# Performance work log

Hardware: AMD Instinct MI355X
Metric: run time of the kernel (lower is better)

Reference implementation:

```python
import jax, jax.numpy as jnp
import numpy as np

L = 4000      # num identities
C = 8         # num cameras; center bank is label-major: center j -> (label j//C, cam j%C)
T = 0.07      # temperature
HARD_NEG_K = 50
LAMDA = 0.5


def setup_inputs() -> dict:
    key = jax.random.key(0)
    k1, k2, k3, k4 = jax.random.split(key, 4)
    n, d = 256, 2048
    feats = jax.random.normal(k1, (n, d), dtype=jnp.float32)
    centers = jax.random.normal(k2, (L * C, d), dtype=jnp.float32)
    centers = centers / jnp.linalg.norm(centers, axis=1, keepdims=True)  # bank is kept unit-norm
    labels = jax.random.randint(k3, (n,), 0, L, dtype=jnp.int64)
    camids = jax.random.randint(k4, (n,), 0, C, dtype=jnp.int64)
    return {"feats": feats, "centers": centers, "labels": labels, "camids": camids, "epoch": 5}


def _cap_losses(feats, centers, labels, camids):
    n = feats.shape[0]
    M = centers.shape[0]
    feats = feats / jnp.linalg.norm(feats, axis=1, keepdims=True)  # F.normalize(p=2, dim=1)
    center_labels = jnp.arange(M) // C
    center_cams = jnp.arange(M) % C

    sims = jnp.einsum('nd,md->nm', feats, centers) / T  # [n, M] scaled similarities
    own_idx = labels * C + camids                        # cam_label_index[(label, cam)]
    own = sims[jnp.arange(n), own_idx]                   # numerator logits
    exp_sims = jnp.exp(sims)                             # unit vectors => sims <= 1/T ~ 14.3, safe

    # ---- intra-camera loss: denominator over centers sharing the sample's camid ----
    cam_mask = (center_cams[None, :] == camids[:, None])
    denom_intra = jnp.sum(exp_sims * cam_mask, axis=1)
    loss_i = own - jnp.log(denom_intra)                  # log(frac_up/frac_down)
    # mean per camid, then sum over camids present in the batch, negated
    ones = jnp.ones((n,), dtype=feats.dtype)
    cam_sums = jax.ops.segment_sum(loss_i, camids, num_segments=C)
    cam_cnts = jax.ops.segment_sum(ones, camids, num_segments=C)
    loss_intra = -jnp.sum(jnp.where(cam_cnts > 0, cam_sums / jnp.maximum(cam_cnts, 1.0), 0.0))

    # ---- inter loss: same-label centers + first-K hard negatives (in bank order) ----
    lbl_mask = (center_labels[None, :] == labels[:, None])
    other = ~lbl_mask
    # torch concatenates other-label centers in label order and takes the FIRST 50 (a slice,
    # not top-k); label-major bank order makes that = first 50 other-label centers by index.
    rank = jnp.cumsum(other.astype(jnp.int32), axis=1)
    hard_mask = other & (rank <= HARD_NEG_K)
    denom_inter = jnp.sum(exp_sims * lbl_mask, axis=1) + jnp.sum(exp_sims * hard_mask, axis=1)
    loss_j = own - jnp.log(denom_inter)
    lbl_sums = jax.ops.segment_sum(loss_j, labels, num_segments=L)
    lbl_cnts = jax.ops.segment_sum(ones, labels, num_segments=L)
    loss_inter = -jnp.sum(jnp.where(lbl_cnts > 0, lbl_sums / jnp.maximum(lbl_cnts, 1.0), 0.0))

    return loss_intra, loss_inter


def reference(feats, centers, labels, camids, epoch):
    loss_intra, loss_inter = _cap_losses(feats, centers, labels, camids)
    if epoch < 5:  # epoch is a static python int
        return loss_intra
    return jnp.stack([loss_intra, LAMDA * loss_inter])
```

## Files before the change

### kernel.cpp

```cpp
#include <hip/hip_runtime.h>

typedef __attribute__((ext_vector_type(8))) __bf16 bf16x8;
typedef __attribute__((ext_vector_type(4))) __bf16 bf16x4;
typedef __attribute__((ext_vector_type(4))) float f32x4;

#define N_SAMP 256
#define DIM    2048
#define NCENT  32000
#define INV_T  14.285714285714285714f
#define NWG    500

__global__ __launch_bounds__(256) void norm_kernel(const float* __restrict__ feats,
                                                   __bf16* __restrict__ fnorm,
                                                   float* __restrict__ d_acc) {
    int row = blockIdx.x;
    int tid = threadIdx.x;
    if (row < 16) d_acc[row * 256 + tid] = 0.f;
    const float* src = feats + (size_t)row * DIM;
    float4 v0 = reinterpret_cast<const float4*>(src)[2 * tid];
    float4 v1 = reinterpret_cast<const float4*>(src)[2 * tid + 1];
    float ss = v0.x * v0.x + v0.y * v0.y + v0.z * v0.z + v0.w * v0.w
             + v1.x * v1.x + v1.y * v1.y + v1.z * v1.z + v1.w * v1.w;
    #pragma unroll
    for (int off = 1; off < 64; off <<= 1) ss += __shfl_xor(ss, off, 64);
    __shared__ float wsum[4];
    if ((tid & 63) == 0) wsum[tid >> 6] = ss;
    __syncthreads();
    float inv = 1.0f / sqrtf(wsum[0] + wsum[1] + wsum[2] + wsum[3]);
    bf16x8 o;
    o[0] = (__bf16)(v0.x * inv); o[1] = (__bf16)(v0.y * inv);
    o[2] = (__bf16)(v0.z * inv); o[3] = (__bf16)(v0.w * inv);
    o[4] = (__bf16)(v1.x * inv); o[5] = (__bf16)(v1.y * inv);
    o[6] = (__bf16)(v1.z * inv); o[7] = (__bf16)(v1.w * inv);
    *reinterpret_cast<bf16x8*>(fnorm + (size_t)row * DIM + tid * 8) = o;
}

__global__ __launch_bounds__(512, 4) void sims_kernel(
    const __bf16* __restrict__ fnorm, const float* __restrict__ centers,
    const int* __restrict__ labels, const int* __restrict__ camids,
    float* __restrict__ d_acc, float* __restrict__ d_own)
{
    __shared__ __align__(16) char sA[2][8192];
    __shared__ __align__(16) char sB[2][8192];

    const int tid  = threadIdx.x;
    const int wave = tid >> 6;
    const int lane = tid & 63;
    const int l15  = lane & 15;
    const int lhi  = lane >> 4;

    const int d   = blockIdx.x;
    const int xcd = d & 7, loc = d >> 3;
    const int lid = (xcd < 4 ? xcd * 63 : 252 + (xcd - 4) * 62) + loc;
    const int nb  = lid >> 1;
    const int mb  = lid & 1;

    const int wr = (wave >> 2) * 64;
    const int wc = (wave & 3) * 32;

    f32x4 acc[4][2] = {};

    const float4* bsrc = reinterpret_cast<const float4*>(centers);
    const uint4*  asrc = reinterpret_cast<const uint4*>(fnorm);

    auto issue = [&](int step, float4& b0, float4& b1, uint4& a) {
        int r0 = tid >> 3, p0 = tid & 7;
        b0 = bsrc[(size_t)(nb * 128 + r0) * 512 + step * 8 + p0];
        int r1 = (512 + tid) >> 3, p1 = tid & 7;
        b1 = bsrc[(size_t)(nb * 128 + r1) * 512 + step * 8 + p1];
        int ra = tid >> 2, pa = tid & 3;
        a = asrc[(size_t)(mb * 128 + ra) * 256 + step * 4 + pa];
    };
    auto wrbuf = [&](int b, const float4& b0, const float4& b1, const uint4& a) {
        #pragma unroll
        for (int j = 0; j < 2; ++j) {
            const float4& v = j ? b1 : b0;
            int row = (j * 512 + tid) >> 3, pos = tid & 7;
            int adr = (row * 64 + pos * 8) ^ ((row & 7) << 4);
            bf16x4 o;
            o[0] = (__bf16)v.x; o[1] = (__bf16)v.y;
            o[2] = (__bf16)v.z; o[3] = (__bf16)v.w;
            *reinterpret_cast<uint2*>(&sB[b][adr]) = __builtin_bit_cast(uint2, o);
        }
        {
            int row = tid >> 2, pos = tid & 3;
            int adr = (row * 64 + pos * 16) ^ ((row & 7) << 4);
            *reinterpret_cast<uint4*>(&sA[b][adr]) = a;
        }
    };
    auto compute = [&](int b) {
        bf16x8 af[4], bf[2];
        #pragma unroll
        for (int mi = 0; mi < 4; ++mi) {
            int row = wr + mi * 16 + l15;
            int adr = (row * 64 + lhi * 16) ^ ((row & 7) << 4);
            af[mi] = *reinterpret_cast<const bf16x8*>(&sA[b][adr]);
        }
        #pragma unroll
        for (int ni = 0; ni < 2; ++ni) {
            int row = wc + ni * 16 + l15;
            int adr = (row * 64 + lhi * 16) ^ ((row & 7) << 4);
            bf[ni] = *reinterpret_cast<const bf16x8*>(&sB[b][adr]);
        }
        #pragma unroll
        for (int mi = 0; mi < 4; ++mi)
            #pragma unroll
            for (int ni = 0; ni < 2; ++ni)
                acc[mi][ni] = __builtin_amdgcn_mfma_f32_16x16x32_bf16(
                    af[mi], bf[ni], acc[mi][ni], 0, 0, 0);
    };
    #define BAR() do { asm volatile("s_waitcnt lgkmcnt(0)" ::: "memory"); \
                       __builtin_amdgcn_s_barrier(); } while (0)

    float4 b0A, b1A; uint4 aA;
    float4 b0B, b1B; uint4 aB;

    issue(0, b0A, b1A, aA);
    issue(1, b0B, b1B, aB);
    wrbuf(0, b0A, b1A, aA);
    BAR();
    for (int t = 0; t < 64; t += 2) {
        if (t + 2 < 64) issue(t + 2, b0A, b1A, aA);
        compute(0);
        wrbuf(1, b0B, b1B, aB);
        BAR();
        if (t + 3 < 64) issue(t + 3, b0B, b1B, aB);
        compute(1);
        if (t + 2 < 64) {
            wrbuf(0, b0A, b1A, aA);
            BAR();
        }
    }

    float* slot = d_acc + (d & 7) * 512;
    #pragma unroll
    for (int mi = 0; mi < 4; ++mi) {
        #pragma unroll
        for (int r = 0; r < 4; ++r) {
            int i   = mb * 128 + wr + mi * 16 + lhi * 4 + r;
            int lab = labels[i], cam = camids[i];
            int oidx = lab * 8 + cam;
            float pi = 0.f, pj = 0.f;
            #pragma unroll
            for (int ni = 0; ni < 2; ++ni) {
                int c = nb * 128 + wc + ni * 16 + l15;
                float s = acc[mi][ni][r] * INV_T;
                float e = __expf(s);
                if ((l15 & 7) == cam) pi += e;
                bool ol = ((c >> 3) == lab);
                bool hard = (!ol) && (c < ((c < lab * 8) ? 50 : 58));
                if (ol || hard) pj += e;
                if (c == oidx) d_own[i] = s;
            }
            #pragma unroll
            for (int off = 1; off < 16; off <<= 1) {
                pi += __shfl_xor(pi, off, 64);
                pj += __shfl_xor(pj, off, 64);
            }
            if (l15 == 0) {
                atomicAdd(&slot[i], pi);
                atomicAdd(&slot[N_SAMP + i], pj);
            }
        }
    }
}

__global__ __launch_bounds__(256) void finalize_kernel(
    const float* __restrict__ d_acc, const float* __restrict__ d_own,
    const int* __restrict__ labels, const int* __restrict__ camids,
    float* __restrict__ out, int out_size)
{
    __shared__ int s_lab[N_SAMP], s_cam[N_SAMP];
    __shared__ float wsum[8];
    int tid = threadIdx.x;
    s_lab[tid] = labels[tid];
    s_cam[tid] = camids[tid];
    __syncthreads();
    int myl = s_lab[tid], myc = s_cam[tid];
    int nl = 0, nc = 0;
    for (int j = 0; j < N_SAMP; ++j) {
        nl += (s_lab[j] == myl);
        nc += (s_cam[j] == myc);
    }
    float di = 0.f, dj = 0.f;
    #pragma unroll
    for (int s = 0; s < 8; ++s) {
        di += d_acc[s * 512 + tid];
        dj += d_acc[s * 512 + 256 + tid];
    }
    float own = d_own[tid];
    float li = own - logf(di);
    float lj = own - logf(dj);
    float a = li / (float)nc;
    float b = lj / (float)nl;
    #pragma unroll
    for (int off = 1; off < 64; off <<= 1) {
        a += __shfl_xor(a, off, 64);
        b += __shfl_xor(b, off, 64);
    }
    if ((tid & 63) == 0) { wsum[tid >> 6] = a; wsum[4 + (tid >> 6)] = b; }
    __syncthreads();
    if (tid == 0) {
        float sa = wsum[0] + wsum[1] + wsum[2] + wsum[3];
        float sb = wsum[4] + wsum[5] + wsum[6] + wsum[7];
        out[0] = -sa;
        if (out_size > 1) out[1] = -0.5f * sb;
    }
}

extern "C" void kernel_launch(void* const* d_in, const int* in_sizes, int n_in,
                              void* d_out, int out_size, void* d_ws, size_t ws_size,
                              hipStream_t stream) {
    const float* feats   = (const float*)d_in[0];
    const float* centers = (const float*)d_in[1];
    const int*   labels  = (const int*)d_in[2];
    const int*   camids  = (const int*)d_in[3];
    float* out = (float*)d_out;

    __bf16* fnorm = (__bf16*)d_ws;
    float* d_acc  = (float*)((char*)d_ws + (size_t)N_SAMP * DIM * sizeof(__bf16));
    float* d_own  = d_acc + 8 * 2 * N_SAMP;

    norm_kernel<<<N_SAMP, 256, 0, stream>>>(feats, fnorm, d_acc);
    sims_kernel<<<NWG, 512, 0, stream>>>(fnorm, centers, labels, camids, d_acc, d_own);
    finalize_kernel<<<1, 256, 0, stream>>>(d_acc, d_own, labels, camids, out, out_size);
}
```

Before: 89.61 us.

## Load A fragments directly from global into registers, bypassing LDS

Drops the shared-memory staging buffer for the normalized feature tile. Each wave now loads its bf16 A fragments straight from global memory into registers one step ahead. This removes the LDS writes and reads for A and halves LDS use. The cost is more global loads, since A rows are now loaded redundantly by the four waves that share them, and more registers held for the prefetched fragments.

```diff
diff --git a/kernel.cpp b/kernel.cpp
--- a/kernel.cpp
+++ b/kernel.cpp
@@ -40,7 +40,6 @@
     const int* __restrict__ labels, const int* __restrict__ camids,
     float* __restrict__ d_acc, float* __restrict__ d_own)
 {
-    __shared__ __align__(16) char sA[2][8192];
     __shared__ __align__(16) char sB[2][8192];
 
     const int tid  = threadIdx.x;
@@ -61,17 +60,21 @@
     f32x4 acc[4][2] = {};
 
     const float4* bsrc = reinterpret_cast<const float4*>(centers);
-    const uint4*  asrc = reinterpret_cast<const uint4*>(fnorm);
-
-    auto issue = [&](int step, float4& b0, float4& b1, uint4& a) {
-        int r0 = tid >> 3, p0 = tid & 7;
-        b0 = bsrc[(size_t)(nb * 128 + r0) * 512 + step * 8 + p0];
-        int r1 = (512 + tid) >> 3, p1 = tid & 7;
-        b1 = bsrc[(size_t)(nb * 128 + r1) * 512 + step * 8 + p1];
-        int ra = tid >> 2, pa = tid & 3;
-        a = asrc[(size_t)(mb * 128 + ra) * 256 + step * 4 + pa];
-    };
-    auto wrbuf = [&](int b, const float4& b0, const float4& b1, const uint4& a) {
+    const __bf16* abase = fnorm + (size_t)(mb * 128 + wr + l15) * DIM + lhi * 8;
+
+    auto issueB = [&](int step, float4& b0, float4& b1) {
+        int r0 = tid >> 3, p = tid & 7;
+        b0 = bsrc[(size_t)(nb * 128 + r0) * 512 + step * 8 + p];
+        int r1 = (512 + tid) >> 3;
+        b1 = bsrc[(size_t)(nb * 128 + r1) * 512 + step * 8 + p];
+    };
+    auto issueA = [&](int step, bf16x8 (&af)[4]) {
+        const __bf16* a0 = abase + step * 32;
+        #pragma unroll
+        for (int mi = 0; mi < 4; ++mi)
+            af[mi] = *reinterpret_cast<const bf16x8*>(a0 + (size_t)mi * 16 * DIM);
+    };
+    auto wrbuf = [&](int b, const float4& b0, const float4& b1) {
         #pragma unroll
         for (int j = 0; j < 2; ++j) {
             const float4& v = j ? b1 : b0;
@@ -82,20 +85,9 @@
             o[2] = (__bf16)v.z; o[3] = (__bf16)v.w;
             *reinterpret_cast<uint2*>(&sB[b][adr]) = __builtin_bit_cast(uint2, o);
         }
-        {
-            int row = tid >> 2, pos = tid & 3;
-            int adr = (row * 64 + pos * 16) ^ ((row & 7) << 4);
-            *reinterpret_cast<uint4*>(&sA[b][adr]) = a;
-        }
-    };
-    auto compute = [&](int b) {
-        bf16x8 af[4], bf[2];
-        #pragma unroll
-        for (int mi = 0; mi < 4; ++mi) {
-            int row = wr + mi * 16 + l15;
-            int adr = (row * 64 + lhi * 16) ^ ((row & 7) << 4);
-            af[mi] = *reinterpret_cast<const bf16x8*>(&sA[b][adr]);
-        }
+    };
+    auto compute = [&](int b, const bf16x8 (&af)[4]) {
+        bf16x8 bf[2];
         #pragma unroll
         for (int ni = 0; ni < 2; ++ni) {
             int row = wc + ni * 16 + l15;
@@ -112,22 +104,25 @@
     #define BAR() do { asm volatile("s_waitcnt lgkmcnt(0)" ::: "memory"); \
                        __builtin_amdgcn_s_barrier(); } while (0)
 
-    float4 b0A, b1A; uint4 aA;
-    float4 b0B, b1B; uint4 aB;
-
-    issue(0, b0A, b1A, aA);
-    issue(1, b0B, b1B, aB);
-    wrbuf(0, b0A, b1A, aA);
+    float4 b0A, b1A, b0B, b1B;
+    bf16x8 afA[4], afB[4];
+
+    issueB(0, b0A, b1A);
+    issueB(1, b0B, b1B);
+    issueA(0, afA);
+    wrbuf(0, b0A, b1A);
     BAR();
     for (int t = 0; t < 64; t += 2) {
-        if (t + 2 < 64) issue(t + 2, b0A, b1A, aA);
-        compute(0);
-        wrbuf(1, b0B, b1B, aB);
+        if (t + 2 < 64) issueB(t + 2, b0A, b1A);
+        issueA(t + 1, afB);
+        compute(0, afA);
+        wrbuf(1, b0B, b1B);
         BAR();
-        if (t + 3 < 64) issue(t + 3, b0B, b1B, aB);
-        compute(1);
+        if (t + 3 < 64) issueB(t + 3, b0B, b1B);
+        if (t + 2 < 64) issueA(t + 2, afA);
+        compute(1, afB);
         if (t + 2 < 64) {
-            wrbuf(0, b0A, b1A, aA);
+            wrbuf(0, b0A, b1A);
             BAR();
         }
     }
```

Result: slower. 160.2 us (+78.8%).

## Tile all 256 samples per workgroup so each center tile is read once

Applied to the files above, without the earlier changes.

Each workgroup now covers all 256 samples against 128 centers, not 128 samples. This halves the workgroup count and removes the duplicated fp32 center loads and bf16 conversions that the two sample-half blocks used to repeat. Each wave now holds a 64x64 accumulator tile (16 MFMA accumulators), and the A buffer doubles in LDS. The cost is lower occupancy (launch bounds of 2 instead of 4), higher register pressure, and only 250 workgroups to spread across the CUs.

```diff
diff --git a/kernel.cpp b/kernel.cpp
--- a/kernel.cpp
+++ b/kernel.cpp
@@ -8,7 +8,7 @@
 #define DIM    2048
 #define NCENT  32000
 #define INV_T  14.285714285714285714f
-#define NWG    500
+#define NWG    250
 
 __global__ __launch_bounds__(256) void norm_kernel(const float* __restrict__ feats,
                                                    __bf16* __restrict__ fnorm,
@@ -35,12 +35,12 @@
     *reinterpret_cast<bf16x8*>(fnorm + (size_t)row * DIM + tid * 8) = o;
 }
 
-__global__ __launch_bounds__(512, 4) void sims_kernel(
+__global__ __launch_bounds__(512, 2) void sims_kernel(
     const __bf16* __restrict__ fnorm, const float* __restrict__ centers,
     const int* __restrict__ labels, const int* __restrict__ camids,
     float* __restrict__ d_acc, float* __restrict__ d_own)
 {
-    __shared__ __align__(16) char sA[2][8192];
+    __shared__ __align__(16) char sA[2][16384];
     __shared__ __align__(16) char sB[2][8192];
 
     const int tid  = threadIdx.x;
@@ -49,47 +49,49 @@
     const int l15  = lane & 15;
     const int lhi  = lane >> 4;
 
-    const int d   = blockIdx.x;
-    const int xcd = d & 7, loc = d >> 3;
-    const int lid = (xcd < 4 ? xcd * 63 : 252 + (xcd - 4) * 62) + loc;
-    const int nb  = lid >> 1;
-    const int mb  = lid & 1;
-
-    const int wr = (wave >> 2) * 64;
-    const int wc = (wave & 3) * 32;
-
-    f32x4 acc[4][2] = {};
+    const int nb    = blockIdx.x;
+    const int cbase = nb * 128;
+
+    const int wr = (wave >> 1) * 64;
+    const int wc = (wave & 1) * 64;
+
+    f32x4 acc[4][4] = {};
 
     const float4* bsrc = reinterpret_cast<const float4*>(centers);
     const uint4*  asrc = reinterpret_cast<const uint4*>(fnorm);
 
-    auto issue = [&](int step, float4& b0, float4& b1, uint4& a) {
-        int r0 = tid >> 3, p0 = tid & 7;
-        b0 = bsrc[(size_t)(nb * 128 + r0) * 512 + step * 8 + p0];
-        int r1 = (512 + tid) >> 3, p1 = tid & 7;
-        b1 = bsrc[(size_t)(nb * 128 + r1) * 512 + step * 8 + p1];
-        int ra = tid >> 2, pa = tid & 3;
-        a = asrc[(size_t)(mb * 128 + ra) * 256 + step * 4 + pa];
+    auto issue = [&](int step, float4& b0, float4& b1, uint4& a0, uint4& a1) {
+        int rb0 = tid >> 3, p = tid & 7;
+        b0 = bsrc[(size_t)(cbase + rb0) * 512 + step * 8 + p];
+        int rb1 = 64 + rb0;
+        b1 = bsrc[(size_t)(cbase + rb1) * 512 + step * 8 + p];
+        int ra0 = tid >> 2, pa = tid & 3;
+        a0 = asrc[(size_t)ra0 * 256 + step * 4 + pa];
+        int ra1 = 128 + ra0;
+        a1 = asrc[(size_t)ra1 * 256 + step * 4 + pa];
     };
-    auto wrbuf = [&](int b, const float4& b0, const float4& b1, const uint4& a) {
+    auto wrbuf = [&](int b, const float4& b0, const float4& b1,
+                     const uint4& a0, const uint4& a1) {
         #pragma unroll
         for (int j = 0; j < 2; ++j) {
             const float4& v = j ? b1 : b0;
-            int row = (j * 512 + tid) >> 3, pos = tid & 7;
+            int row = j * 64 + (tid >> 3), pos = tid & 7;
             int adr = (row * 64 + pos * 8) ^ ((row & 7) << 4);
             bf16x4 o;
             o[0] = (__bf16)v.x; o[1] = (__bf16)v.y;
             o[2] = (__bf16)v.z; o[3] = (__bf16)v.w;
             *reinterpret_cast<uint2*>(&sB[b][adr]) = __builtin_bit_cast(uint2, o);
         }
-        {
-            int row = tid >> 2, pos = tid & 3;
+        #pragma unroll
+        for (int j = 0; j < 2; ++j) {
+            const uint4& v = j ? a1 : a0;
+            int row = j * 128 + (tid >> 2), pos = tid & 3;
             int adr = (row * 64 + pos * 16) ^ ((row & 7) << 4);
-            *reinterpret_cast<uint4*>(&sA[b][adr]) = a;
+            *reinterpret_cast<uint4*>(&sA[b][adr]) = v;
         }
     };
     auto compute = [&](int b) {
-        bf16x8 af[4], bf[2];
+        bf16x8 af[4], bf[4];
         #pragma unroll
         for (int mi = 0; mi < 4; ++mi) {
             int row = wr + mi * 16 + l15;
@@ -97,7 +99,7 @@
             af[mi] = *reinterpret_cast<const bf16x8*>(&sA[b][adr]);
         }
         #pragma unroll
-        for (int ni = 0; ni < 2; ++ni) {
+        for (int ni = 0; ni < 4; ++ni) {
             int row = wc + ni * 16 + l15;
             int adr = (row * 64 + lhi * 16) ^ ((row & 7) << 4);
             bf[ni] = *reinterpret_cast<const bf16x8*>(&sB[b][adr]);
@@ -105,45 +107,45 @@
         #pragma unroll
         for (int mi = 0; mi < 4; ++mi)
             #pragma unroll
-            for (int ni = 0; ni < 2; ++ni)
+            for (int ni = 0; ni < 4; ++ni)
                 acc[mi][ni] = __builtin_amdgcn_mfma_f32_16x16x32_bf16(
                     af[mi], bf[ni], acc[mi][ni], 0, 0, 0);
     };
     #define BAR() do { asm volatile("s_waitcnt lgkmcnt(0)" ::: "memory"); \
                        __builtin_amdgcn_s_barrier(); } while (0)
 
-    float4 b0A, b1A; uint4 aA;
-    float4 b0B, b1B; uint4 aB;
-
-    issue(0, b0A, b1A, aA);
-    issue(1, b0B, b1B, aB);
-    wrbuf(0, b0A, b1A, aA);
+    float4 b0A, b1A, b0B, b1B;
+    uint4  a0A, a1A, a0B, a1B;
+
+    issue(0, b0A, b1A, a0A, a1A);
+    issue(1, b0B, b1B, a0B, a1B);
+    wrbuf(0, b0A, b1A, a0A, a1A);
     BAR();
     for (int t = 0; t < 64; t += 2) {
-        if (t + 2 < 64) issue(t + 2, b0A, b1A, aA);
+        if (t + 2 < 64) issue(t + 2, b0A, b1A, a0A, a1A);
         compute(0);
-        wrbuf(1, b0B, b1B, aB);
+        wrbuf(1, b0B, b1B, a0B, a1B);
         BAR();
-        if (t + 3 < 64) issue(t + 3, b0B, b1B, aB);
+        if (t + 3 < 64) issue(t + 3, b0B, b1B, a0B, a1B);
         compute(1);
         if (t + 2 < 64) {
-            wrbuf(0, b0A, b1A, aA);
+            wrbuf(0, b0A, b1A, a0A, a1A);
             BAR();
         }
     }
 
-    float* slot = d_acc + (d & 7) * 512;
+    float* slot = d_acc + (nb & 7) * 512;
     #pragma unroll
     for (int mi = 0; mi < 4; ++mi) {
         #pragma unroll
         for (int r = 0; r < 4; ++r) {
-            int i   = mb * 128 + wr + mi * 16 + lhi * 4 + r;
+            int i   = wr + mi * 16 + lhi * 4 + r;
             int lab = labels[i], cam = camids[i];
             int oidx = lab * 8 + cam;
             float pi = 0.f, pj = 0.f;
             #pragma unroll
-            for (int ni = 0; ni < 2; ++ni) {
-                int c = nb * 128 + wc + ni * 16 + l15;
+            for (int ni = 0; ni < 4; ++ni) {
+                int c = cbase + wc + ni * 16 + l15;
                 float s = acc[mi][ni][r] * INV_T;
                 float e = __expf(s);
                 if ((l15 & 7) == cam) pi += e;
```

Result: faster. 86.05 us (-4.0%).
